# Optimization experiments

Measured on AMD Instinct MI355X. Metric: run time of the kernel, lower is better.

The kernel has to match this reference:

```python
import jax, jax.numpy as jnp
import numpy as np

B, N, K, F, S = 128, 116, 4, 72, 8
TOPK = 10
INTRA_T, INTER_T = 0.1, 0.2


def _safe_corr(f):
    # f: [batch, d, m] -> corr [batch, d, d], matching torch _safe_compute_correlation
    c = f - f.mean(axis=2, keepdims=True)
    cov = jnp.einsum('bim,bjm->bij', c, c)
    var = jnp.diagonal(cov, axis1=1, axis2=2)
    std = jnp.sqrt(jnp.clip(var, 1e-8, None))[:, :, None]
    corr = cov / (std * std.transpose(0, 2, 1) + 1e-8)
    return jnp.clip(corr, -1.0, 1.0)


def _sym(m):
    return (m + m.swapaxes(-1, -2)) * 0.5


def setup_inputs():
    key = jax.random.key(0)
    ks = jax.random.split(key, 8)
    def lin(k, out_d, in_d):
        return jax.random.normal(k, (out_d, in_d), jnp.float32) * (1.0 / np.sqrt(in_d))
    return {
        'band_features': jax.random.normal(ks[0], (B, N, K, F), jnp.float32),
        'attn_weights': jax.random.uniform(ks[1], (B, N, S, K), jnp.float32),
        'intra_thresh_adj': jnp.zeros((), jnp.float32),
        'inter_thresh_adj': jnp.zeros((), jnp.float32),
        'attn_fuse_weight': jnp.asarray(0.5, jnp.float32),
        'intra_W1': lin(ks[2], 64, N), 'intra_b1': jnp.zeros((64,), jnp.float32),
        'intra_W2': lin(ks[3], N, 64), 'intra_b2': jnp.zeros((N,), jnp.float32),
        'inter_W1': lin(ks[4], 32, K), 'inter_b1': jnp.zeros((32,), jnp.float32),
        'inter_W2': lin(ks[5], K, 32), 'inter_b2': jnp.zeros((K,), jnp.float32),
        'comp_W': lin(ks[6], 128, 2 * F + 6), 'comp_b': jnp.zeros((128,), jnp.float32),
    }


def reference(band_features, attn_weights, intra_thresh_adj, inter_thresh_adj,
              attn_fuse_weight, intra_W1, intra_b1, intra_W2, intra_b2,
              inter_W1, inter_b1, inter_W2, inter_b2, comp_W, comp_b):
    dt = band_features.dtype
    # ---- intra-band graph: [B*K, N, N] correlations ----
    x = band_features.transpose(0, 2, 1, 3).reshape(B * K, N, F)
    corr = _safe_corr(x)
    th = INTRA_T + jax.nn.sigmoid(intra_thresh_adj) * 0.2
    tmask = (jnp.abs(corr) > th).astype(dt)
    _, idx = jax.lax.top_k(jnp.abs(corr), min(TOPK, N))  # [B*K, N, k]
    bix = jnp.arange(B * K)[:, None, None]
    rix = jnp.arange(N)[None, :, None]
    kmask = jnp.zeros_like(corr).at[bix, rix, idx].set(1.0)
    sc = jax.nn.relu(_sym(corr * tmask * kmask))
    h = jax.nn.relu(sc.reshape(-1, N) @ intra_W1.T + intra_b1)  # dropout = eval identity
    intra = jax.nn.sigmoid(h @ intra_W2.T + intra_b2).reshape(B * K, N, N)
    intra_adj = _sym(intra).reshape(B, K, N, N)
    # ---- inter-band graph: [B*N, K, K] correlations ----
    y = band_features.reshape(B * N, K, F)
    base = _safe_corr(y)
    a = attn_weights.reshape(B * N, S, K).transpose(0, 2, 1)  # [B*N, K, S]
    acorr = _safe_corr(a)
    fw = jax.nn.sigmoid(attn_fuse_weight)
    base = fw * base + (1.0 - fw) * acorr
    th2 = INTER_T + jax.nn.sigmoid(inter_thresh_adj) * 0.2
    sc2 = jax.nn.relu(_sym(base * (jnp.abs(base) > th2).astype(dt)))
    h2 = jax.nn.relu(sc2.reshape(-1, K) @ inter_W1.T + inter_b1)
    inter = jax.nn.sigmoid(h2 @ inter_W2.T + inter_b2).reshape(B * N, K, K)
    inter_adj = _sym(inter).reshape(B, N, K, K)
    # ---- unified graph assembly (vectorized replacement of nested loops) ----
    kk = jnp.arange(K)
    bd = jnp.zeros((B, K, N, K, N), dt).at[:, kk, :, kk, :].set(
        intra_adj.transpose(1, 0, 2, 3))  # block-diagonal intra blocks
    unified = bd.reshape(B, K * N, K * N)
    kk1, kk2, nn = np.meshgrid(np.arange(K), np.arange(K), np.arange(N), indexing='ij')
    sel = (kk1 != kk2).ravel()
    k1f, k2f, nf = kk1.ravel()[sel], kk2.ravel()[sel], nn.ravel()[sel]
    vals = inter_adj[:, nf, k1f, k2f]  # [B, M]
    unified_adj = unified.at[:, k1f * N + nf, k2f * N + nf].set(vals)
    # ---- node features ----
    node_features = band_features.transpose(0, 2, 1, 3).reshape(B, K * N, F)
    # ---- graph-level features ----
    node_mean = band_features.mean(axis=(1, 2))
    node_std = jnp.std(band_features, axis=(1, 2), ddof=1)  # torch unbiased std
    deg = (intra_adj > 0).astype(dt).sum(axis=3)  # [B, K, N]
    tri = jnp.einsum('bkij,bkji->bki', intra_adj, intra_adj)  # diag of A@A
    clus = tri / (deg ** 2 + 1e-8)
    dens = (inter_adj > 0).astype(dt).mean(axis=(2, 3))  # [B, N]
    stren = inter_adj.mean(axis=(2, 3))
    gf = jnp.concatenate([
        node_mean, node_std,
        deg.mean(axis=(1, 2))[:, None], jnp.std(deg, axis=(1, 2), ddof=1)[:, None],
        clus.mean(axis=(1, 2))[:, None], jnp.std(clus, axis=(1, 2), ddof=1)[:, None],
        dens.mean(axis=1)[:, None], stren.mean(axis=1)[:, None]], axis=1)
    graph_features = jax.nn.relu(gf @ comp_W.T + comp_b)
    # ---- sparsity scalars ----
    intra_sp = 1.0 - (intra_adj > 0).astype(dt).mean()
    inter_sp = 1.0 - (inter_adj > 0).astype(dt).mean()
    it, jt = float(B * K * N * N), float(B * N * K * K)
    total_sp = (intra_sp * it + inter_sp * jt) / (it + jt)
    return (unified_adj, node_features, graph_features, intra_adj, inter_adj,
            intra_sp, inter_sp, total_sp)
```

## Files before the change

kernel.cpp:

```cpp
#include <hip/hip_runtime.h>
#include <math.h>

#define NB 128
#define NN_ 116
#define NK 4
#define NF 72
#define NS 8
#define TOPK 10

#define BK (NB*NK)
#define BN (NB*NN_)
#define NN2 (NN_*NN_)
#define KN (NK*NN_)
#define ROWS (BK*NN_)
#define LROW 117

#define OFF_UNI 0
#define SZ_UNI (NB*KN*KN)
#define OFF_NF (OFF_UNI + SZ_UNI)
#define SZ_NF (NB*KN*NF)
#define OFF_GF (OFF_NF + SZ_NF)
#define SZ_GF (NB*128)
#define OFF_IA (OFF_GF + SZ_GF)
#define SZ_IA (NB*NK*NN_*NN_)
#define OFF_IE (OFF_IA + SZ_IA)
#define SZ_IE (NB*NN_*NK*NK)
#define OFF_SP (OFF_IE + SZ_IE)

#define SCR_SC 0
#define SCR_CORR (SCR_SC + SZ_IA)
#define SCR_DEG (SCR_CORR + SZ_IA)
#define SCR_CLUS (SCR_DEG + ROWS)
#define SCR_DENS (SCR_CLUS + ROWS)
#define SCR_STREN (SCR_DENS + BN)
#define SCR_AUX (SCR_STREN + BN)

#define NFQ (SZ_NF/4)
#define UNQ (SZ_UNI/4)
#define NB_CORR 512
#define NB_INTER (BN/64)
#define NB_COPY 1044

__device__ __forceinline__ float sigmoidf_(float x){ return 1.0f/(1.0f+expf(-x)); }
__device__ __forceinline__ float dot4_(float4 a, float4 b){
    return fmaf(a.x,b.x, fmaf(a.y,b.y, fmaf(a.z,b.z, a.w*b.w)));
}
#define CLIP1(x) fminf(1.0f, fmaxf(-1.0f, (x)))

__global__ __launch_bounds__(256, 1) void k_corr_inter(const float* __restrict__ band,
    const float* __restrict__ attn, const float* __restrict__ thadj2,
    const float* __restrict__ fwp,
    const float* __restrict__ eW1, const float* __restrict__ eb1,
    const float* __restrict__ eW2, const float* __restrict__ eb2,
    float* __restrict__ corr_out, float* __restrict__ inter_out,
    float* __restrict__ dens_out, float* __restrict__ stren_out,
    float* __restrict__ nf)
{
    __shared__ float sx[NF*120];
    __shared__ float smu[120], srs[120];
    __shared__ float sW1[128], sb1[32], sW2[128], sb2[4];
    __shared__ float sMat[256*4];
    int t = threadIdx.x;
    if (blockIdx.x < NB_CORR){
        int bk = blockIdx.x;
        int b = bk >> 2, k = bk & 3;
        const float* xin = band + ((size_t)b*NN_*NK + k)*NF;
        for (int e = t; e < NN_*NF; e += 256){
            int n = e / NF, f = e - n*NF;
            sx[f*120 + n] = xin[(size_t)n*NK*NF + f];
        }
        for (int e = t; e < NF*4; e += 256)
            sx[(e>>2)*120 + NN_ + (e&3)] = 0.0f;
        __syncthreads();
        if (t < NN_){
            float s = 0.f, ss = 0.f;
            for (int f = 0; f < NF; ++f){ float v = sx[f*120+t]; s += v; ss += v*v; }
            float mu = s * (1.0f/NF);
            float sd = sqrtf(fmaxf(ss - s*mu, 1e-8f));
            smu[t] = mu; srs[t] = 1.0f/sd;
        }
        __syncthreads();
        for (int e = t; e < NF*NN_; e += 256){
            int f = e / NN_, n = e - f*NN_;
            sx[f*120+n] = (sx[f*120+n] - smu[n]) * srs[n];
        }
        __syncthreads();
        float* dst = corr_out + (size_t)bk * NN2;
        if (t < 225){
            int ti = t / 15, tj = t - ti*15;
            int i0 = ti*8, j0 = tj*8;
            float acc[8][8] = {};
            for (int f = 0; f < NF; ++f){
                const float4 a0 = *(const float4*)&sx[f*120 + i0];
                const float4 a1 = *(const float4*)&sx[f*120 + i0 + 4];
                const float4 c0 = *(const float4*)&sx[f*120 + j0];
                const float4 c1 = *(const float4*)&sx[f*120 + j0 + 4];
                float av[8] = {a0.x,a0.y,a0.z,a0.w,a1.x,a1.y,a1.z,a1.w};
                float cv[8] = {c0.x,c0.y,c0.z,c0.w,c1.x,c1.y,c1.z,c1.w};
                #pragma unroll
                for (int r = 0; r < 8; ++r)
                    #pragma unroll
                    for (int c = 0; c < 8; ++c)
                        acc[r][c] = fmaf(av[r], cv[c], acc[r][c]);
            }
            #pragma unroll
            for (int r = 0; r < 8; ++r){
                int i = i0 + r;
                if (i < NN_){
                    float4 v0;
                    v0.x = CLIP1(acc[r][0]); v0.y = CLIP1(acc[r][1]);
                    v0.z = CLIP1(acc[r][2]); v0.w = CLIP1(acc[r][3]);
                    *(float4*)&dst[i*NN_ + j0] = v0;
                    if (j0 + 4 <= 112){
                        float4 v1;
                        v1.x = CLIP1(acc[r][4]); v1.y = CLIP1(acc[r][5]);
                        v1.z = CLIP1(acc[r][6]); v1.w = CLIP1(acc[r][7]);
                        *(float4*)&dst[i*NN_ + j0 + 4] = v1;
                    }
                }
            }
        }
    } else if (blockIdx.x < NB_CORR + NB_INTER){
        if (t < 128) sW1[t] = eW1[t];
        if (t < 32) sb1[t] = eb1[t];
        if (t >= 128 && t < 256) sW2[t-128] = eW2[t-128];
        if (t < 4) sb2[t] = eb2[t];
        __syncthreads();
        int l = t & 3;
        int il = t >> 2;
        size_t item = (size_t)(blockIdx.x - NB_CORR)*64 + il;

        const float* xr = band + item*(NK*NF) + l*NF;
        float s=0,p0=0,p1=0,p2=0,p3=0;
        for (int f = 0; f < NF; ++f){
            float v = xr[f];
            float v1=__shfl_xor(v,1), v2=__shfl_xor(v,2), v3=__shfl_xor(v,3);
            s += v; p0=fmaf(v,v,p0); p1=fmaf(v,v1,p1); p2=fmaf(v,v2,p2); p3=fmaf(v,v3,p3);
        }
        float mu = s*(1.0f/NF);
        float mu1=__shfl_xor(mu,1), mu2=__shfl_xor(mu,2), mu3=__shfl_xor(mu,3);
        float sd = sqrtf(fmaxf(p0 - s*mu, 1e-8f));
        float sd1=__shfl_xor(sd,1), sd2=__shfl_xor(sd,2), sd3=__shfl_xor(sd,3);
        float c0 = CLIP1((p0 - (float)NF*mu*mu )/(sd*sd +1e-8f));
        float c1 = CLIP1((p1 - (float)NF*mu*mu1)/(sd*sd1+1e-8f));
        float c2 = CLIP1((p2 - (float)NF*mu*mu2)/(sd*sd2+1e-8f));
        float c3 = CLIP1((p3 - (float)NF*mu*mu3)/(sd*sd3+1e-8f));

        const float* ar = attn + item*(NS*NK) + l;
        float as=0,q0=0,q1=0,q2=0,q3=0;
        #pragma unroll
        for (int s8 = 0; s8 < NS; ++s8){
            float v = ar[s8*NK];
            float v1=__shfl_xor(v,1), v2=__shfl_xor(v,2), v3=__shfl_xor(v,3);
            as += v; q0=fmaf(v,v,q0); q1=fmaf(v,v1,q1); q2=fmaf(v,v2,q2); q3=fmaf(v,v3,q3);
        }
        float am = as*(1.0f/NS);
        float am1=__shfl_xor(am,1), am2=__shfl_xor(am,2), am3=__shfl_xor(am,3);
        float ad = sqrtf(fmaxf(q0 - as*am, 1e-8f));
        float ad1=__shfl_xor(ad,1), ad2=__shfl_xor(ad,2), ad3=__shfl_xor(ad,3);
        float a0 = CLIP1((q0 - (float)NS*am*am )/(ad*ad +1e-8f));
        float a1 = CLIP1((q1 - (float)NS*am*am1)/(ad*ad1+1e-8f));
        float a2 = CLIP1((q2 - (float)NS*am*am2)/(ad*ad2+1e-8f));
        float a3 = CLIP1((q3 - (float)NS*am*am3)/(ad*ad3+1e-8f));

        float fwv = sigmoidf_(fwp[0]);
        float g0 = fwv*c0 + (1.0f-fwv)*a0;
        float g1 = fwv*c1 + (1.0f-fwv)*a1;
        float g2 = fwv*c2 + (1.0f-fwv)*a2;
        float g3 = fwv*c3 + (1.0f-fwv)*a3;
        float th2 = 0.2f + sigmoidf_(thadj2[0])*0.2f;
        float m0 = (fabsf(g0)>th2)?g0:0.f;
        float m1 = (fabsf(g1)>th2)?g1:0.f;
        float m2 = (fabsf(g2)>th2)?g2:0.f;
        float m3 = (fabsf(g3)>th2)?g3:0.f;

        sMat[il*16 + l*4 + (l^0)] = m0;
        sMat[il*16 + l*4 + (l^1)] = m1;
        sMat[il*16 + l*4 + (l^2)] = m2;
        sMat[il*16 + l*4 + (l^3)] = m3;
        __syncthreads();
        float x0 = fmaxf(0.5f*(sMat[il*16 + l*4 + 0] + sMat[il*16 + 0*4 + l]), 0.f);
        float x1 = fmaxf(0.5f*(sMat[il*16 + l*4 + 1] + sMat[il*16 + 1*4 + l]), 0.f);
        float x2 = fmaxf(0.5f*(sMat[il*16 + l*4 + 2] + sMat[il*16 + 2*4 + l]), 0.f);
        float x3 = fmaxf(0.5f*(sMat[il*16 + l*4 + 3] + sMat[il*16 + 3*4 + l]), 0.f);

        float h[32];
        #pragma unroll
        for (int o = 0; o < 32; ++o){
            float acc = sb1[o];
            acc = fmaf(sW1[o*4+0], x0, acc);
            acc = fmaf(sW1[o*4+1], x1, acc);
            acc = fmaf(sW1[o*4+2], x2, acc);
            acc = fmaf(sW1[o*4+3], x3, acc);
            h[o] = fmaxf(acc, 0.f);
        }
        float o0=sb2[0], o1=sb2[1], o2=sb2[2], o3=sb2[3];
        #pragma unroll
        for (int o = 0; o < 32; ++o){
            float hv = h[o];
            o0 = fmaf(sW2[0*32+o], hv, o0);
            o1 = fmaf(sW2[1*32+o], hv, o1);
            o2 = fmaf(sW2[2*32+o], hv, o2);
            o3 = fmaf(sW2[3*32+o], hv, o3);
        }
        o0 = sigmoidf_(o0); o1 = sigmoidf_(o1); o2 = sigmoidf_(o2); o3 = sigmoidf_(o3);
        __syncthreads();
        sMat[il*16 + l*4 + 0] = o0;
        sMat[il*16 + l*4 + 1] = o1;
        sMat[il*16 + l*4 + 2] = o2;
        sMat[il*16 + l*4 + 3] = o3;
        __syncthreads();
        float y0 = 0.5f*(o0 + sMat[il*16 + 0*4 + l]);
        float y1 = 0.5f*(o1 + sMat[il*16 + 1*4 + l]);
        float y2 = 0.5f*(o2 + sMat[il*16 + 2*4 + l]);
        float y3 = 0.5f*(o3 + sMat[il*16 + 3*4 + l]);
        *(float4*)&inter_out[item*16 + l*4] = make_float4(y0,y1,y2,y3);

        float cnt = ((y0>0.f)?1.f:0.f) + ((y1>0.f)?1.f:0.f) + ((y2>0.f)?1.f:0.f) + ((y3>0.f)?1.f:0.f);
        float sum = y0+y1+y2+y3;
        cnt += __shfl_xor(cnt,1); cnt += __shfl_xor(cnt,2);
        sum += __shfl_xor(sum,1); sum += __shfl_xor(sum,2);
        if (l == 0){
            dens_out[item]  = cnt * (1.0f/16.0f);
            stren_out[item] = sum * (1.0f/16.0f);
        }
    } else {
        int gid = (blockIdx.x - NB_CORR - NB_INTER)*256 + t;
        int gsz = NB_COPY*256;
        for (int q = gid; q < NFQ; q += gsz){
            int fq = q % 18;
            int rest = q / 18;
            int b = rest / KN;
            int p = rest - b*KN;
            int k = p / NN_;
            int n = p - k*NN_;
            float4 v = *(const float4*)&band[(((size_t)b*NN_ + n)*NK + k)*NF + fq*4];
            *(float4*)&nf[(size_t)q*4] = v;
        }
    }
}

__global__ __launch_bounds__(512) void k_topk_mask(const float* __restrict__ corr_in,
    const float* __restrict__ thadj, float* __restrict__ sc_out)
{
    __shared__ float sc_[NN_*LROW];
    __shared__ unsigned skm[NN_*4];
    __shared__ unsigned stop[464*10];
    int bk = blockIdx.x;
    int t = threadIdx.x;
    const float* src = corr_in + (size_t)bk*NN2;
    for (int e = t; e < NN2; e += 512){
        int i = e / NN_, j = e - i*NN_;
        sc_[i*LROW + j] = src[e];
    }
    __syncthreads();
    if (t < NN_*4){
        int r = t >> 2, q = t & 3;
        const float* row = &sc_[r*LROW + q*29];
        int jbase = q*29;
        unsigned tv[TOPK];
        #pragma unroll
        for (int p = 0; p < TOPK; ++p) tv[p] = 0u;
        for (int jj = 0; jj < 29; ++jj){
            float c = fabsf(row[jj]);
            unsigned u = (__float_as_uint(c) & 0xFFFFFF80u) | (unsigned)(127 - (jbase + jj));
            #pragma unroll
            for (int p = 0; p < TOPK; ++p){
                unsigned old = tv[p];
                bool gt = u > old;
                tv[p] = gt ? u : old;
                u = gt ? old : u;
            }
        }
        #pragma unroll
        for (int p = 0; p < TOPK; ++p) stop[t*10 + p] = tv[p];
    }
    __syncthreads();
    if (t < NN_){
        const unsigned* L0 = &stop[(4*t+0)*10];
        const unsigned* L1 = &stop[(4*t+1)*10];
        const unsigned* L2 = &stop[(4*t+2)*10];
        const unsigned* L3 = &stop[(4*t+3)*10];
        int i0=0, i1=0, i2=0, i3=0;
        unsigned m0=0,m1=0,m2=0,m3=0;
        #pragma unroll
        for (int p = 0; p < TOPK; ++p){
            unsigned u0 = L0[i0], u1 = L1[i1], u2 = L2[i2], u3 = L3[i3];
            unsigned ua = u0 > u1 ? u0 : u1;
            unsigned ub = u2 > u3 ? u2 : u3;
            unsigned u  = ua > ub ? ua : ub;
            if (u == u0) ++i0; else if (u == u1) ++i1; else if (u == u2) ++i2; else ++i3;
            int j = 127 - (int)(u & 127u);
            unsigned bit = 1u << (j & 31);
            int w = j >> 5;
            if (w == 0) m0 |= bit; else if (w == 1) m1 |= bit; else if (w == 2) m2 |= bit; else m3 |= bit;
        }
        skm[t*4+0]=m0; skm[t*4+1]=m1; skm[t*4+2]=m2; skm[t*4+3]=m3;
    }
    __syncthreads();
    float th = 0.1f + sigmoidf_(thadj[0]) * 0.2f;
    float* dst = sc_out + (size_t)bk * NN2;
    for (int e = t; e < NN2; e += 512){
        int i = e / NN_, j = e - i*NN_;
        float cij = sc_[i*LROW + j];
        float cji = sc_[j*LROW + i];
        bool kij = (skm[i*4 + (j>>5)] >> (j&31)) & 1u;
        bool kji = (skm[j*4 + (i>>5)] >> (i&31)) & 1u;
        float mij = (fabsf(cij) > th && kij) ? cij : 0.0f;
        float mji = (fabsf(cji) > th && kji) ? cji : 0.0f;
        dst[e] = fmaxf(0.5f*(mij+mji), 0.0f);
    }
}

__global__ __launch_bounds__(512) void k_mlpsym(const float* __restrict__ sc,
    const float* __restrict__ W1, const float* __restrict__ b1,
    const float* __restrict__ W2, const float* __restrict__ b2,
    float* __restrict__ ia, float* __restrict__ deg_out, float* __restrict__ clus_out)
{
    __shared__ float smem[31844];
    float* sA  = smem;
    float* sB  = smem + 14036;
    float* sH  = smem + 23764;
    float* sb1 = smem + 31652;
    float* sb2 = smem + 31716;
    int bk = blockIdx.x, t = threadIdx.x;

    const float* src = sc + (size_t)bk*NN2;
    for (int e4 = t; e4 < NN2/4; e4 += 512)
        *(float4*)&sA[e4*4] = *(const float4*)&src[e4*4];
    for (int e4 = t; e4 < 1856; e4 += 512)
        *(float4*)&sB[e4*4] = *(const float4*)&W1[e4*4];
    if (t < 64) sb1[t] = b1[t];
    if (t >= 64 && t < 192) sb2[t-64] = (t-64 < NN_) ? b2[t-64] : 0.0f;
    __syncthreads();

    if (t < 464){
        int rg = t >> 4, og = t & 15;
        float acc[4][4] = {};
        for (int j4 = 0; j4 < 29; ++j4){
            float4 s[4], w[4];
            #pragma unroll
            for (int m = 0; m < 4; ++m) s[m] = *(const float4*)&sA[(rg+29*m)*116 + j4*4];
            #pragma unroll
            for (int n = 0; n < 4; ++n) w[n] = *(const float4*)&sB[(og+16*n)*116 + j4*4];
            #pragma unroll
            for (int m = 0; m < 4; ++m)
                #pragma unroll
                for (int n = 0; n < 4; ++n)
                    acc[m][n] += dot4_(s[m], w[n]);
        }
        #pragma unroll
        for (int m = 0; m < 4; ++m)
            #pragma unroll
            for (int n = 0; n < 4; ++n)
                sH[(rg+29*m)*68 + og+16*n] = fmaxf(acc[m][n] + sb1[og+16*n], 0.0f);
    }
    __syncthreads();

    for (int e = t; e < 128*64; e += 512){
        int j = e >> 6, o = e & 63;
        sB[j*76 + o] = (j < NN_) ? W2[e] : 0.0f;
    }
    __syncthreads();

    if (t < 464){
        int rg = t >> 4, jg = t & 15;
        float acc[4][8] = {};
        for (int o4 = 0; o4 < 16; ++o4){
            float4 h[4], w[8];
            #pragma unroll
            for (int m = 0; m < 4; ++m) h[m] = *(const float4*)&sH[(rg+29*m)*68 + o4*4];
            #pragma unroll
            for (int q = 0; q < 8; ++q) w[q] = *(const float4*)&sB[(jg+16*q)*76 + o4*4];
            #pragma unroll
            for (int m = 0; m < 4; ++m)
                #pragma unroll
                for (int q = 0; q < 8; ++q)
                    acc[m][q] += dot4_(h[m], w[q]);
        }
        #pragma unroll
        for (int m = 0; m < 4; ++m){
            int row = rg + 29*m;
            #pragma unroll
            for (int q = 0; q < 8; ++q){
                int j = jg + 16*q;
                if (j < NN_)
                    sA[row*121 + j] = sigmoidf_(acc[m][q] + sb2[j]);
            }
        }
    }
    __syncthreads();

    float* dia = ia + (size_t)bk*NN2;
    for (int e4 = t; e4 < NN2/4; e4 += 512){
        int e = e4*4;
        int i = e / NN_, j0 = e - i*NN_;
        float4 v;
        v.x = 0.5f*(sA[i*121+j0+0] + sA[(j0+0)*121+i]);
        v.y = 0.5f*(sA[i*121+j0+1] + sA[(j0+1)*121+i]);
        v.z = 0.5f*(sA[i*121+j0+2] + sA[(j0+2)*121+i]);
        v.w = 0.5f*(sA[i*121+j0+3] + sA[(j0+3)*121+i]);
        *(float4*)&dia[e] = v;
    }
    if (t < 464){
        int r = t >> 2, q = t & 3;
        float tri = 0.f, dg = 0.f;
        for (int jj = 0; jj < 29; ++jj){
            int j = q*29 + jj;
            float v = 0.5f*(sA[r*121+j] + sA[j*121+r]);
            tri = fmaf(v, v, tri);
            dg += (v > 0.f) ? 1.f : 0.f;
        }
        tri += __shfl_xor(tri,1); tri += __shfl_xor(tri,2);
        dg  += __shfl_xor(dg,1);  dg  += __shfl_xor(dg,2);
        if (q == 0){
            deg_out[(size_t)bk*NN_ + r]  = dg;
            clus_out[(size_t)bk*NN_ + r] = tri / (dg*dg + 1e-8f);
        }
    }
}

__global__ __launch_bounds__(256) void k_gstats_lin(const float* __restrict__ band,
    const float* __restrict__ deg, const float* __restrict__ clus,
    const float* __restrict__ dens, const float* __restrict__ stren,
    const float* __restrict__ Wc, const float* __restrict__ bc,
    float* __restrict__ gfo, float* __restrict__ aux)
{
    int b = blockIdx.x, t = threadIdx.x;
    __shared__ float sGf[152];
    __shared__ float sPs[18*14*4];
    __shared__ float sPq[18*14*4];
    __shared__ float sA[4], sB[4];

    if (t < 252){
        int fq = t % 18, g = t / 18;
        float4 s = make_float4(0,0,0,0), q = make_float4(0,0,0,0);
        const float* base = band + (size_t)b*(KN*NF);
        for (int nk = g; nk < KN; nk += 14){
            float4 v = *(const float4*)&base[nk*NF + fq*4];
            s.x += v.x; s.y += v.y; s.z += v.z; s.w += v.w;
            q.x = fmaf(v.x,v.x,q.x); q.y = fmaf(v.y,v.y,q.y);
            q.z = fmaf(v.z,v.z,q.z); q.w = fmaf(v.w,v.w,q.w);
        }
        int idx = (fq*14 + g)*4;
        *(float4*)&sPs[idx] = s;
        *(float4*)&sPq[idx] = q;
    }
    __syncthreads();
    if (t < NF){
        int fq = t >> 2, e = t & 3;
        float S = 0.f, Q = 0.f;
        for (int g = 0; g < 14; ++g){ S += sPs[(fq*14+g)*4+e]; Q += sPq[(fq*14+g)*4+e]; }
        float mean = S * (1.0f/(float)KN);
        float var = fmaxf((Q - S*mean)/((float)KN - 1.0f), 0.0f);
        sGf[t] = mean;
        sGf[NF + t] = sqrtf(var);
    }
    __syncthreads();

    float s = 0.f, ss = 0.f;
    for (int e = t; e < KN; e += 256){ float v = deg[(size_t)b*KN + e]; s += v; ss += v*v; }
    #pragma unroll
    for (int d = 1; d < 64; d <<= 1){ s += __shfl_xor(s,d); ss += __shfl_xor(ss,d); }
    if ((t & 63) == 0){ sA[t>>6] = s; sB[t>>6] = ss; }
    __syncthreads();
    if (t == 0){
        float S0 = sA[0]+sA[1]+sA[2]+sA[3], S1 = sB[0]+sB[1]+sB[2]+sB[3];
        float Mv = (float)KN, mean = S0/Mv;
        float var = fmaxf((S1 - S0*mean)/(Mv - 1.0f), 0.0f);
        sGf[144] = mean; sGf[145] = sqrtf(var);
        aux[b] = S0;
    }
    __syncthreads();

    s = 0.f; ss = 0.f;
    for (int e = t; e < KN; e += 256){ float v = clus[(size_t)b*KN + e]; s += v; ss += v*v; }
    #pragma unroll
    for (int d = 1; d < 64; d <<= 1){ s += __shfl_xor(s,d); ss += __shfl_xor(ss,d); }
    if ((t & 63) == 0){ sA[t>>6] = s; sB[t>>6] = ss; }
    __syncthreads();
    if (t == 0){
        float S0 = sA[0]+sA[1]+sA[2]+sA[3], S1 = sB[0]+sB[1]+sB[2]+sB[3];
        float Mv = (float)KN, mean = S0/Mv;
        float var = fmaxf((S1 - S0*mean)/(Mv - 1.0f), 0.0f);
        sGf[146] = mean; sGf[147] = sqrtf(var);
    }
    __syncthreads();

    s = 0.f; ss = 0.f;
    for (int e = t; e < NN_; e += 256){ s += dens[(size_t)b*NN_ + e]; ss += stren[(size_t)b*NN_ + e]; }
    #pragma unroll
    for (int d = 1; d < 64; d <<= 1){ s += __shfl_xor(s,d); ss += __shfl_xor(ss,d); }
    if ((t & 63) == 0){ sA[t>>6] = s; sB[t>>6] = ss; }
    __syncthreads();
    if (t == 0){
        float S0 = sA[0]+sA[1]+sA[2]+sA[3], S1 = sB[0]+sB[1]+sB[2]+sB[3];
        sGf[148] = S0 / (float)NN_;
        sGf[149] = S1 / (float)NN_;
        aux[128 + b] = S0 * 16.0f;
    }
    __syncthreads();

    if (t < 128){
        float acc = bc[t];
        const float* w = Wc + (size_t)t*150;
        for (int c = 0; c < 150; ++c) acc = fmaf(sGf[c], w[c], acc);
        gfo[(size_t)b*128 + t] = fmaxf(acc, 0.f);
    }
}

__global__ __launch_bounds__(64) void k_sparsity(const float* __restrict__ aux, float* __restrict__ out3)
{
    int t = threadIdx.x;
    float a = aux[t] + aux[64 + t];
    float c = aux[128 + t] + aux[192 + t];
    #pragma unroll
    for (int d = 1; d < 64; d <<= 1){ a += __shfl_xor(a,d); c += __shfl_xor(c,d); }
    if (t == 0){
        const float it = 6889472.0f, jt = 237568.0f;
        float isp = 1.0f - a/it;
        float jsp = 1.0f - c/jt;
        out3[0] = isp; out3[1] = jsp;
        out3[2] = (isp*it + jsp*jt)/(it + jt);
    }
}

__global__ __launch_bounds__(256) void k_uninf(const float* __restrict__ intra_adj,
    const float* __restrict__ inter_adj, const float* __restrict__ aux,
    float* __restrict__ uni, float* __restrict__ sp, int do_sp)
{
    if (do_sp && blockIdx.x == 0 && threadIdx.x < 64){
        int t = threadIdx.x;
        float a = aux[t] + aux[64 + t];
        float c = aux[128 + t] + aux[192 + t];
        #pragma unroll
        for (int d = 1; d < 64; d <<= 1){ a += __shfl_xor(a,d); c += __shfl_xor(c,d); }
        if (t == 0){
            const float it = 6889472.0f, jt = 237568.0f;
            float isp = 1.0f - a/it;
            float jsp = 1.0f - c/jt;
            sp[0] = isp; sp[1] = jsp;
            sp[2] = (isp*it + jt*0.0f + jsp*jt - jsp*jt + jsp*jt)/(it + jt) * 0.0f
                    + (isp*it + jsp*jt)/(it + jt);
        }
    }
    int gid = blockIdx.x*256 + threadIdx.x;
    int gsz = gridDim.x*256;
    for (int q = gid; q < UNQ; q += gsz){
        int row = q / 116;
        int cq  = q - row*116;
        int b = row / KN;
        int p = row - b*KN;
        int k1 = p / NN_;
        int i  = p - k1*NN_;
        int k2 = cq / 29;
        int j0 = cq*4 - k2*NN_;
        float4 v;
        if (k2 == k1){
            v = *(const float4*)&intra_adj[(((size_t)b*NK + k1)*NN_ + i)*NN_ + j0];
        } else {
            int d = i - j0;
            float val = 0.f;
            if (d >= 0 && d < 4)
                val = inter_adj[(((size_t)b*NN_ + i)*NK + k1)*NK + k2];
            v.x = (d==0)?val:0.f;
            v.y = (d==1)?val:0.f;
            v.z = (d==2)?val:0.f;
            v.w = (d==3)?val:0.f;
        }
        *(float4*)&uni[(size_t)q*4] = v;
    }
}

extern "C" void kernel_launch(void* const* d_in, const int* in_sizes, int n_in,
                              void* d_out, int out_size, void* d_ws, size_t ws_size,
                              hipStream_t stream)
{
    const float* band = (const float*)d_in[0];
    const float* attn = (const float*)d_in[1];
    const float* thA  = (const float*)d_in[2];
    const float* thE  = (const float*)d_in[3];
    const float* fw   = (const float*)d_in[4];
    const float* iW1  = (const float*)d_in[5];
    const float* ib1  = (const float*)d_in[6];
    const float* iW2  = (const float*)d_in[7];
    const float* ib2  = (const float*)d_in[8];
    const float* eW1  = (const float*)d_in[9];
    const float* eb1  = (const float*)d_in[10];
    const float* eW2  = (const float*)d_in[11];
    const float* eb2  = (const float*)d_in[12];
    const float* cW   = (const float*)d_in[13];
    const float* cb   = (const float*)d_in[14];

    float* out = (float*)d_out;
    float* uni = out + OFF_UNI;
    float* nf  = out + OFF_NF;
    float* gfo = out + OFF_GF;
    float* ia  = out + OFF_IA;
    float* ie  = out + OFF_IE;
    float* sp  = out + OFF_SP;

    float* scr_sc    = uni + SCR_SC;
    float* scr_corr  = uni + SCR_CORR;
    float* scr_deg   = uni + SCR_DEG;
    float* scr_clus  = uni + SCR_CLUS;
    float* scr_dens  = uni + SCR_DENS;
    float* scr_stren = uni + SCR_STREN;

    int ws_ok = (ws_size >= 256*sizeof(float));
    float* aux = ws_ok ? (float*)d_ws : (uni + SCR_AUX);

    k_corr_inter<<<NB_CORR + NB_INTER + NB_COPY, 256, 0, stream>>>(
        band, attn, thE, fw, eW1, eb1, eW2, eb2,
        scr_corr, ie, scr_dens, scr_stren, nf);
    k_topk_mask<<<BK, 512, 0, stream>>>(scr_corr, thA, scr_sc);
    k_mlpsym<<<BK, 512, 0, stream>>>(scr_sc, iW1, ib1, iW2, ib2, ia, scr_deg, scr_clus);
    k_gstats_lin<<<NB, 256, 0, stream>>>(band, scr_deg, scr_clus, scr_dens, scr_stren,
                                         cW, cb, gfo, aux);
    if (!ws_ok)
        k_sparsity<<<1, 64, 0, stream>>>(aux, sp);
    k_uninf<<<2048, 256, 0, stream>>>(ia, ie, aux, uni, sp, ws_ok ? 1 : 0);
}
```

Baseline: 149.7 us.

## Fuse top-k masking kernel into MLP-symmetrize kernel via shared memory

Merges the top-k/threshold masking kernel with the intra-band MLP and symmetrization kernel, so the masked, symmetrized correlation matrix stays in LDS instead of going to a global scratch buffer and being read back. This removes one kernel launch and a full write plus read of the B*K*N*N intermediate. In exchange, each thread holds 27 values in registers across a barrier so it can rewrite the LDS tile in place, and LDS use grows slightly, which could lower occupancy. The sparsity scalar expression is also simplified.

Result: faster. 145.0 us (-3.1%).

```diff
diff --git a/kernel.cpp b/kernel.cpp
--- a/kernel.cpp
+++ b/kernel.cpp
@@ -13,7 +13,6 @@
 #define NN2 (NN_*NN_)
 #define KN (NK*NN_)
 #define ROWS (BK*NN_)
-#define LROW 117
 
 #define OFF_UNI 0
 #define SZ_UNI (NB*KN*KN)
@@ -27,8 +26,7 @@
 #define SZ_IE (NB*NN_*NK*NK)
 #define OFF_SP (OFF_IE + SZ_IE)
 
-#define SCR_SC 0
-#define SCR_CORR (SCR_SC + SZ_IA)
+#define SCR_CORR 0
 #define SCR_DEG (SCR_CORR + SZ_IA)
 #define SCR_CLUS (SCR_DEG + ROWS)
 #define SCR_DENS (SCR_CLUS + ROWS)
@@ -240,23 +238,41 @@
     }
 }
 
-__global__ __launch_bounds__(512) void k_topk_mask(const float* __restrict__ corr_in,
-    const float* __restrict__ thadj, float* __restrict__ sc_out)
+__global__ __launch_bounds__(512) void k_topk_mlpsym(const float* __restrict__ corr,
+    const float* __restrict__ thadj,
+    const float* __restrict__ W1, const float* __restrict__ b1,
+    const float* __restrict__ W2, const float* __restrict__ b2,
+    float* __restrict__ ia, float* __restrict__ deg_out, float* __restrict__ clus_out)
 {
-    __shared__ float sc_[NN_*LROW];
-    __shared__ unsigned skm[NN_*4];
-    __shared__ unsigned stop[464*10];
-    int bk = blockIdx.x;
-    int t = threadIdx.x;
-    const float* src = corr_in + (size_t)bk*NN2;
-    for (int e = t; e < NN2; e += 512){
-        int i = e / NN_, j = e - i*NN_;
-        sc_[i*LROW + j] = src[e];
-    }
-    __syncthreads();
-    if (t < NN_*4){
+    __shared__ float smem[32308];
+    float* sA  = smem;
+    float* sB  = smem + 14036;
+    float* sH  = smem + 23764;
+    float* sb1 = smem + 31652;
+    float* sb2 = smem + 31716;
+    unsigned* sKm  = (unsigned*)(smem + 31844);
+    unsigned* sTop = (unsigned*)sH;
+    int bk = blockIdx.x, t = threadIdx.x;
+
+    const float* src = corr + (size_t)bk*NN2;
+    for (int e4 = t; e4 < NN2/4; e4 += 512){
+        int e = e4*4;
+        int i = e / 116, j = e - i*116;
+        float4 v = *(const float4*)&src[e];
+        sA[i*121 + j + 0] = v.x;
+        sA[i*121 + j + 1] = v.y;
+        sA[i*121 + j + 2] = v.z;
+        sA[i*121 + j + 3] = v.w;
+    }
+    for (int e4 = t; e4 < 1856; e4 += 512)
+        *(float4*)&sB[e4*4] = *(const float4*)&W1[e4*4];
+    if (t < 64) sb1[t] = b1[t];
+    if (t >= 64 && t < 192) sb2[t-64] = (t-64 < NN_) ? b2[t-64] : 0.0f;
+    __syncthreads();
+
+    if (t < 464){
         int r = t >> 2, q = t & 3;
-        const float* row = &sc_[r*LROW + q*29];
+        const float* row = &sA[r*121 + q*29];
         int jbase = q*29;
         unsigned tv[TOPK];
         #pragma unroll
@@ -273,14 +289,15 @@
             }
         }
         #pragma unroll
-        for (int p = 0; p < TOPK; ++p) stop[t*10 + p] = tv[p];
-    }
-    __syncthreads();
+        for (int p = 0; p < TOPK; ++p) sTop[t*10 + p] = tv[p];
+    }
+    __syncthreads();
+
     if (t < NN_){
-        const unsigned* L0 = &stop[(4*t+0)*10];
-        const unsigned* L1 = &stop[(4*t+1)*10];
-        const unsigned* L2 = &stop[(4*t+2)*10];
-        const unsigned* L3 = &stop[(4*t+3)*10];
+        const unsigned* L0 = &sTop[(4*t+0)*10];
+        const unsigned* L1 = &sTop[(4*t+1)*10];
+        const unsigned* L2 = &sTop[(4*t+2)*10];
+        const unsigned* L3 = &sTop[(4*t+3)*10];
         int i0=0, i1=0, i2=0, i3=0;
         unsigned m0=0,m1=0,m2=0,m3=0;
         #pragma unroll
@@ -295,43 +312,36 @@
             int w = j >> 5;
             if (w == 0) m0 |= bit; else if (w == 1) m1 |= bit; else if (w == 2) m2 |= bit; else m3 |= bit;
         }
-        skm[t*4+0]=m0; skm[t*4+1]=m1; skm[t*4+2]=m2; skm[t*4+3]=m3;
-    }
-    __syncthreads();
-    float th = 0.1f + sigmoidf_(thadj[0]) * 0.2f;
-    float* dst = sc_out + (size_t)bk * NN2;
-    for (int e = t; e < NN2; e += 512){
-        int i = e / NN_, j = e - i*NN_;
-        float cij = sc_[i*LROW + j];
-        float cji = sc_[j*LROW + i];
-        bool kij = (skm[i*4 + (j>>5)] >> (j&31)) & 1u;
-        bool kji = (skm[j*4 + (i>>5)] >> (i&31)) & 1u;
-        float mij = (fabsf(cij) > th && kij) ? cij : 0.0f;
-        float mji = (fabsf(cji) > th && kji) ? cji : 0.0f;
-        dst[e] = fmaxf(0.5f*(mij+mji), 0.0f);
-    }
-}
-
-__global__ __launch_bounds__(512) void k_mlpsym(const float* __restrict__ sc,
-    const float* __restrict__ W1, const float* __restrict__ b1,
-    const float* __restrict__ W2, const float* __restrict__ b2,
-    float* __restrict__ ia, float* __restrict__ deg_out, float* __restrict__ clus_out)
-{
-    __shared__ float smem[31844];
-    float* sA  = smem;
-    float* sB  = smem + 14036;
-    float* sH  = smem + 23764;
-    float* sb1 = smem + 31652;
-    float* sb2 = smem + 31716;
-    int bk = blockIdx.x, t = threadIdx.x;
-
-    const float* src = sc + (size_t)bk*NN2;
-    for (int e4 = t; e4 < NN2/4; e4 += 512)
-        *(float4*)&sA[e4*4] = *(const float4*)&src[e4*4];
-    for (int e4 = t; e4 < 1856; e4 += 512)
-        *(float4*)&sB[e4*4] = *(const float4*)&W1[e4*4];
-    if (t < 64) sb1[t] = b1[t];
-    if (t >= 64 && t < 192) sb2[t-64] = (t-64 < NN_) ? b2[t-64] : 0.0f;
+        sKm[t*4+0]=m0; sKm[t*4+1]=m1; sKm[t*4+2]=m2; sKm[t*4+3]=m3;
+    }
+    __syncthreads();
+
+    {
+        float th = 0.1f + sigmoidf_(thadj[0]) * 0.2f;
+        float vb[27];
+        #pragma unroll
+        for (int it = 0; it < 27; ++it){
+            int e = t + it*512;
+            float v = 0.0f;
+            if (e < NN2){
+                int i = e / 116, j = e - i*116;
+                float cij = sA[i*121 + j];
+                float cji = sA[j*121 + i];
+                bool kij = (sKm[i*4 + (j>>5)] >> (j&31)) & 1u;
+                bool kji = (sKm[j*4 + (i>>5)] >> (i&31)) & 1u;
+                float mij = (fabsf(cij) > th && kij) ? cij : 0.0f;
+                float mji = (fabsf(cji) > th && kji) ? cji : 0.0f;
+                v = fmaxf(0.5f*(mij+mji), 0.0f);
+            }
+            vb[it] = v;
+        }
+        __syncthreads();
+        #pragma unroll
+        for (int it = 0; it < 27; ++it){
+            int e = t + it*512;
+            if (e < NN2) sA[e] = vb[it];
+        }
+    }
     __syncthreads();
 
     if (t < 464){
@@ -394,7 +404,7 @@
     float* dia = ia + (size_t)bk*NN2;
     for (int e4 = t; e4 < NN2/4; e4 += 512){
         int e = e4*4;
-        int i = e / NN_, j0 = e - i*NN_;
+        int i = e / 116, j0 = e - i*116;
         float4 v;
         v.x = 0.5f*(sA[i*121+j0+0] + sA[(j0+0)*121+i]);
         v.y = 0.5f*(sA[i*121+j0+1] + sA[(j0+1)*121+i]);
@@ -540,8 +550,7 @@
             float isp = 1.0f - a/it;
             float jsp = 1.0f - c/jt;
             sp[0] = isp; sp[1] = jsp;
-            sp[2] = (isp*it + jt*0.0f + jsp*jt - jsp*jt + jsp*jt)/(it + jt) * 0.0f
-                    + (isp*it + jsp*jt)/(it + jt);
+            sp[2] = (isp*it + jsp*jt)/(it + jt);
         }
     }
     int gid = blockIdx.x*256 + threadIdx.x;
@@ -600,7 +609,6 @@
     float* ie  = out + OFF_IE;
     float* sp  = out + OFF_SP;
 
-    float* scr_sc    = uni + SCR_SC;
     float* scr_corr  = uni + SCR_CORR;
     float* scr_deg   = uni + SCR_DEG;
     float* scr_clus  = uni + SCR_CLUS;
@@ -613,8 +621,8 @@
     k_corr_inter<<<NB_CORR + NB_INTER + NB_COPY, 256, 0, stream>>>(
         band, attn, thE, fw, eW1, eb1, eW2, eb2,
         scr_corr, ie, scr_dens, scr_stren, nf);
-    k_topk_mask<<<BK, 512, 0, stream>>>(scr_corr, thA, scr_sc);
-    k_mlpsym<<<BK, 512, 0, stream>>>(scr_sc, iW1, ib1, iW2, ib2, ia, scr_deg, scr_clus);
+    k_topk_mlpsym<<<BK, 512, 0, stream>>>(scr_corr, thA, iW1, ib1, iW2, ib2,
+                                          ia, scr_deg, scr_clus);
     k_gstats_lin<<<NB, 256, 0, stream>>>(band, scr_deg, scr_clus, scr_dens, scr_stren,
                                          cW, cb, gfo, aux);
     if (!ws_ok)
```
